# Optimization experiments

Measured on AMD Instinct MI355X. Metric: run time of the kernel, lower is better.

The kernel has to match this reference:

```python
import jax, jax.numpy as jnp
import numpy as np

N, E, IN, H, OUT, L = 50000, 640000, 64, 128, 128, 4
EPS = 1e-8


def setup_inputs() -> dict:
    key = jax.random.key(0)
    ks = jax.random.split(key, 14)
    rn = lambda k, shp: (jax.random.normal(k, shp, jnp.float32) * 0.05)
    return {
        "h": jax.random.normal(ks[0], (N, IN), jnp.float32),
        "pos": jax.random.normal(ks[1], (N, 3), jnp.float32),
        "edge_index": jax.random.randint(ks[2], (2, E), 0, N),
        "emb_W": rn(ks[3], (IN, H)), "emb_b": jnp.zeros((H,), jnp.float32),
        "msg_W1": rn(ks[4], (L, 2 * H + 1, H)), "msg_b1": jnp.zeros((L, H), jnp.float32),
        "msg_W2": rn(ks[5], (L, H, H)), "msg_b2": jnp.zeros((L, H), jnp.float32),
        "coord_W1": rn(ks[6], (L, H, H)), "coord_b1": jnp.zeros((L, H), jnp.float32),
        "coord_W2": rn(ks[7], (L, H, 1)), "coord_b2": jnp.zeros((L, 1), jnp.float32),
        "node_W1": rn(ks[8], (L, 2 * H, H)), "node_b1": jnp.zeros((L, H), jnp.float32),
        "node_W2": rn(ks[9], (L, H, H)), "node_b2": jnp.zeros((L, H), jnp.float32),
        "out_W1": rn(ks[10], (H, H)), "out_b1": jnp.zeros((H,), jnp.float32),
        "out_W2": rn(ks[11], (H, OUT)), "out_b2": jnp.zeros((OUT,), jnp.float32),
    }


def _egnn_forward(h, pos, src, dst, emb_W, emb_b, msg_W1, msg_b1, msg_W2, msg_b2,
                  coord_W1, coord_b1, coord_W2, coord_b2, node_W1, node_b1,
                  node_W2, node_b2, out_W1, out_b1, out_W2, out_b2):
    n = h.shape[0]
    h = h @ emb_W + emb_b  # node embedding [N, H]
    for l in range(L):
        hi, hj = h[dst], h[src]                     # target i, source j gathers [Etot, H]
        rel = pos[src] - pos[dst]                   # row - col (used for coord update)
        dist = jnp.linalg.norm(rel, axis=-1, keepdims=True)  # symmetric, same as |pos_i - pos_j|
        # message MLP: Linear -> SiLU -> Linear -> SiLU on [h_i, h_j, dist]
        m = jax.nn.silu(jnp.concatenate([hi, hj, dist], axis=-1) @ msg_W1[l] + msg_b1[l])
        m = jax.nn.silu(m @ msg_W2[l] + msg_b2[l])
        agg = jax.ops.segment_sum(m, dst, num_segments=n)  # scatter-add to targets
        # coord update: weights from h[row]=h_j, scatter to col=dst
        w = jax.nn.silu(hj @ coord_W1[l] + coord_b1[l]) @ coord_W2[l] + coord_b2[l]  # [Etot,1]
        coord_diff = w * rel / (dist + EPS)
        pos = pos + jax.ops.segment_sum(coord_diff, dst, num_segments=n)
        # node update with residual
        nh = jax.nn.silu(jnp.concatenate([h, agg], axis=-1) @ node_W1[l] + node_b1[l]) @ node_W2[l] + node_b2[l]
        h = h + nh
    out = jax.nn.silu(h @ out_W1 + out_b1) @ out_W2 + out_b2
    return out, pos


def reference(h, pos, edge_index, emb_W, emb_b, msg_W1, msg_b1, msg_W2, msg_b2,
              coord_W1, coord_b1, coord_W2, coord_b2, node_W1, node_b1,
              node_W2, node_b2, out_W1, out_b1, out_W2, out_b2):
    n = h.shape[0]
    loops = jnp.arange(n)  # add_self_loops
    src = jnp.concatenate([edge_index[0], loops])
    dst = jnp.concatenate([edge_index[1], loops])
    return _egnn_forward(h, pos, src, dst, emb_W, emb_b, msg_W1, msg_b1, msg_W2,
                         msg_b2, coord_W1, coord_b1, coord_W2, coord_b2, node_W1,
                         node_b1, node_W2, node_b2, out_W1, out_b1, out_W2, out_b2)
```

## Files before the change

### kernel.cpp

```cpp
#include <hip/hip_runtime.h>
#include <hip/hip_bf16.h>

#define EPSV 1e-8f

typedef short bf16x8 __attribute__((ext_vector_type(8)));
typedef float f32x4  __attribute__((ext_vector_type(4)));

__device__ __forceinline__ float silu_f(float x) {
    return x * __builtin_amdgcn_rcpf(1.0f + __expf(-x));
}
__device__ __forceinline__ float bf2f(short v) {
    return __uint_as_float(((unsigned int)(unsigned short)v) << 16);
}
__device__ __forceinline__ short f2bfs(float f) {
    __hip_bfloat16 h = __float2bfloat16(f);
    return *(short*)&h;
}

#define MAXM 24
struct PackArgs {
    const float* src[MAXM];
    unsigned int doff[MAXM];
    int nchunk[MAXM];
    int nmat;
};

__global__ __launch_bounds__(256) void repack_kernel(PackArgs pa, __hip_bfloat16* base)
{
    int bid = blockIdx.x;
    int m = 0, c = bid;
    while (m < pa.nmat && c >= pa.nchunk[m]) { c -= pa.nchunk[m]; ++m; }
    const float* src = pa.src[m];
    __hip_bfloat16* dst = base + pa.doff[m] + (size_t)c * 4096;
    for (int o = threadIdx.x; o < 4096; o += 256) {
        int j = o & 7, n = (o >> 3) & 127, g = o >> 10;
        dst[o] = __float2bfloat16(src[(size_t)(c * 32 + g * 8 + j) * 128 + n]);
    }
}

__global__ __launch_bounds__(256) void hist_kernel(
    const int* __restrict__ ei, int* __restrict__ cnt, int E, int N)
{
    int e = blockIdx.x * 256 + threadIdx.x;
    int Etot = E + N;
    if (e < Etot) {
        int d = (e < E) ? ei[E + e] : (e - E);
        atomicAdd(&cnt[d], 1);
    }
}

__global__ __launch_bounds__(256) void scan_block_kernel(
    const int* __restrict__ cnt, int* __restrict__ off, int* __restrict__ part, int n)
{
    __shared__ int sdata[256];
    const int tid = threadIdx.x;
    const int base = blockIdx.x * 4096 + tid * 16;
    int loc[16]; int s = 0;
    #pragma unroll
    for (int i = 0; i < 16; ++i) {
        int idx = base + i;
        int v = (idx < n) ? cnt[idx] : 0;
        loc[i] = s; s += v;
    }
    sdata[tid] = s;
    __syncthreads();
    for (int st = 1; st < 256; st <<= 1) {
        int v = (tid >= st) ? sdata[tid - st] : 0;
        __syncthreads();
        sdata[tid] += v;
        __syncthreads();
    }
    int texc = (tid > 0) ? sdata[tid - 1] : 0;
    #pragma unroll
    for (int i = 0; i < 16; ++i) {
        int idx = base + i;
        if (idx < n) off[idx] = texc + loc[i];
    }
    if (tid == 255) part[blockIdx.x] = sdata[255];
}

__global__ void scan_part_kernel(int* part, int np)
{
    if (threadIdx.x == 0 && blockIdx.x == 0) {
        int run = 0;
        for (int i = 0; i < np; ++i) { int v = part[i]; part[i] = run; run += v; }
    }
}

__global__ __launch_bounds__(256) void scan_add_kernel(
    int* __restrict__ off, const int* __restrict__ part, int n)
{
    int idx = blockIdx.x * 4096 + threadIdx.x * 16;
    int p = part[blockIdx.x];
    #pragma unroll
    for (int i = 0; i < 16; ++i)
        if (idx + i < n) off[idx + i] += p;
}

__global__ __launch_bounds__(256) void scatter_kernel(
    const int* __restrict__ ei, int* __restrict__ off,
    int* __restrict__ esrc, int* __restrict__ edst, int E, int N)
{
    int e = blockIdx.x * 256 + threadIdx.x;
    int Etot = E + N;
    if (e < Etot) {
        int s, d;
        if (e < E) { s = ei[e]; d = ei[E + e]; }
        else       { s = d = e - E; }
        int p = atomicAdd(&off[d], 1);
        esrc[p] = s; edst[p] = d;
    }
}

template<int LDA>
__device__ __forceinline__ void mfma_gemm(const __hip_bfloat16 (*At)[LDA], int acol0,
                                          const __hip_bfloat16* __restrict__ Bp,
                                          int kchunks, int w, int lane, f32x4 acc[4][2])
{
    const int ar = lane & 15, g = lane >> 4;
    const int bc = w * 32 + (lane & 15);
    for (int c = 0; c < kchunks; ++c) {
        const int ao = acol0 + c * 32 + g * 8;
        bf16x8 a0 = *(const bf16x8*)&At[ar +  0][ao];
        bf16x8 a1 = *(const bf16x8*)&At[ar + 16][ao];
        bf16x8 a2 = *(const bf16x8*)&At[ar + 32][ao];
        bf16x8 a3 = *(const bf16x8*)&At[ar + 48][ao];
        const __hip_bfloat16* bb = Bp + ((size_t)((c * 4 + g) * 128) + bc) * 8;
        bf16x8 b0 = *(const bf16x8*)(bb);
        bf16x8 b1 = *(const bf16x8*)(bb + 128);
        acc[0][0] = __builtin_amdgcn_mfma_f32_16x16x32_bf16(a0, b0, acc[0][0], 0, 0, 0);
        acc[1][0] = __builtin_amdgcn_mfma_f32_16x16x32_bf16(a1, b0, acc[1][0], 0, 0, 0);
        acc[2][0] = __builtin_amdgcn_mfma_f32_16x16x32_bf16(a2, b0, acc[2][0], 0, 0, 0);
        acc[3][0] = __builtin_amdgcn_mfma_f32_16x16x32_bf16(a3, b0, acc[3][0], 0, 0, 0);
        acc[0][1] = __builtin_amdgcn_mfma_f32_16x16x32_bf16(a0, b1, acc[0][1], 0, 0, 0);
        acc[1][1] = __builtin_amdgcn_mfma_f32_16x16x32_bf16(a1, b1, acc[1][1], 0, 0, 0);
        acc[2][1] = __builtin_amdgcn_mfma_f32_16x16x32_bf16(a2, b1, acc[2][1], 0, 0, 0);
        acc[3][1] = __builtin_amdgcn_mfma_f32_16x16x32_bf16(a3, b1, acc[3][1], 0, 0, 0);
    }
}

__device__ __forceinline__ void zacc(f32x4 acc[4][2]) {
    #pragma unroll
    for (int r = 0; r < 4; ++r)
        #pragma unroll
        for (int c = 0; c < 2; ++c) acc[r][c] = (f32x4){0.f, 0.f, 0.f, 0.f};
}

__global__ __launch_bounds__(256) void embed_pre_kernel(
    const float* __restrict__ hin,
    const __hip_bfloat16* __restrict__ embWp, const float* __restrict__ embb,
    const __hip_bfloat16* __restrict__ W1p, const float* __restrict__ b1,
    const __hip_bfloat16* __restrict__ cW1p,
    const float* __restrict__ cb1, const float* __restrict__ cW2,
    const float* __restrict__ cb2,
    float* __restrict__ hbuf, __hip_bfloat16* __restrict__ h16,
    __hip_bfloat16* __restrict__ U16, __hip_bfloat16* __restrict__ V16,
    float* __restrict__ wnum, int N)
{
    __shared__ __hip_bfloat16 a_e[64][72];
    __shared__ __hip_bfloat16 a_h[64][136];
    __shared__ float redw[64][4];
    const int t = threadIdx.x;
    const int nb = blockIdx.x * 64;
    const int lane = t & 63, w = t >> 6, g = lane >> 4, l15 = lane & 15;

    #pragma unroll
    for (int it = 0; it < 2; ++it) {
        int flat = t + 256 * it;
        int c8 = flat & 7, e = flat >> 3;
        int node = nb + e; if (node >= N) node = N - 1;
        const float* hp = hin + (size_t)node * 64 + c8 * 8;
        float4 v0 = *(const float4*)hp, v1 = *(const float4*)(hp + 4);
        bf16x8 r;
        r[0] = f2bfs(v0.x); r[1] = f2bfs(v0.y); r[2] = f2bfs(v0.z); r[3] = f2bfs(v0.w);
        r[4] = f2bfs(v1.x); r[5] = f2bfs(v1.y); r[6] = f2bfs(v1.z); r[7] = f2bfs(v1.w);
        *(bf16x8*)(&a_e[e][c8 * 8]) = r;
    }
    __syncthreads();

    const int colA = w * 32 + l15, colB = colA + 16;
    f32x4 acc[4][2];

    zacc(acc);
    mfma_gemm<72>(a_e, 0, embWp, 2, w, lane, acc);
    {
        float bA = embb[colA], bB = embb[colB];
        #pragma unroll
        for (int r = 0; r < 4; ++r)
            #pragma unroll
            for (int q = 0; q < 4; ++q) {
                int row = r * 16 + g * 4 + q;
                int node = nb + row;
                float va = acc[r][0][q] + bA, vb = acc[r][1][q] + bB;
                __hip_bfloat16 ha = __float2bfloat16(va), hb = __float2bfloat16(vb);
                a_h[row][colA] = ha; a_h[row][colB] = hb;
                if (node < N) {
                    size_t off = (size_t)node * 128;
                    hbuf[off + colA] = va; hbuf[off + colB] = vb;
                    h16[off + colA] = ha; h16[off + colB] = hb;
                }
            }
    }
    __syncthreads();

    zacc(acc);
    mfma_gemm<136>(a_h, 0, W1p, 4, w, lane, acc);
    {
        float bA = b1[colA], bB = b1[colB];
        #pragma unroll
        for (int r = 0; r < 4; ++r)
            #pragma unroll
            for (int q = 0; q < 4; ++q) {
                int node = nb + r * 16 + g * 4 + q;
                if (node < N) {
                    U16[(size_t)node * 128 + colA] = __float2bfloat16(acc[r][0][q] + bA);
                    U16[(size_t)node * 128 + colB] = __float2bfloat16(acc[r][1][q] + bB);
                }
            }
    }
    zacc(acc);
    mfma_gemm<136>(a_h, 0, W1p + 4 * 4096, 4, w, lane, acc);
    #pragma unroll
    for (int r = 0; r < 4; ++r)
        #pragma unroll
        for (int q = 0; q < 4; ++q) {
            int node = nb + r * 16 + g * 4 + q;
            if (node < N) {
                V16[(size_t)node * 128 + colA] = __float2bfloat16(acc[r][0][q]);
                V16[(size_t)node * 128 + colB] = __float2bfloat16(acc[r][1][q]);
            }
        }
    zacc(acc);
    mfma_gemm<136>(a_h, 0, cW1p, 4, w, lane, acc);
    {
        float cb1A = cb1[colA], cb1B = cb1[colB];
        float wA = cW2[colA], wB = cW2[colB];
        #pragma unroll
        for (int r = 0; r < 4; ++r)
            #pragma unroll
            for (int q = 0; q < 4; ++q) {
                float p = silu_f(acc[r][0][q] + cb1A) * wA
                        + silu_f(acc[r][1][q] + cb1B) * wB;
                p += __shfl_xor(p, 1);
                p += __shfl_xor(p, 2);
                p += __shfl_xor(p, 4);
                p += __shfl_xor(p, 8);
                if (l15 == 0) redw[r * 16 + g * 4 + q][w] = p;
            }
    }
    __syncthreads();
    if (t < 64 && nb + t < N)
        wnum[nb + t] = redw[t][0] + redw[t][1] + redw[t][2] + redw[t][3] + cb2[0];
}

__global__ __launch_bounds__(256) void edge_kernel(
    const __hip_bfloat16* __restrict__ U16, const __hip_bfloat16* __restrict__ V16,
    const float* __restrict__ wnum, const float* __restrict__ posb,
    const int* __restrict__ esrc, const int* __restrict__ edst,
    const float* __restrict__ W1tail,
    const __hip_bfloat16* __restrict__ W2p, const float* __restrict__ b2,
    float* __restrict__ agg, float* __restrict__ pdel, int Etot)
{
    __shared__ __hip_bfloat16 m1s[64][136];
    __shared__ int   dstl[64];
    __shared__ float relt[3][64], distl[64], wscl[64];

    const int t = threadIdx.x;
    const int eb = blockIdx.x * 64;
    const int lane = t & 63, w = t >> 6, g = lane >> 4, l15 = lane & 15;

    const int c8 = t & 15, row0 = t >> 4;
    bf16x8 uvr[4], vvr[4];
    int dval[4];
    #pragma unroll
    for (int j = 0; j < 4; ++j) {
        int row = row0 + 16 * j;
        int e = eb + row;
        int s = 0, d = 0;
        if (e < Etot) { s = esrc[e]; d = edst[e]; dval[j] = 1; }
        else          { dval[j] = 0; }
        uvr[j] = *(const bf16x8*)(U16 + (size_t)d * 128 + c8 * 8);
        vvr[j] = *(const bf16x8*)(V16 + (size_t)s * 128 + c8 * 8);
    }

    if (t < 64) {
        int e = eb + t;
        int s = 0, d = -1;
        if (e < Etot) { s = esrc[e]; d = edst[e]; }
        dstl[t] = d;
        int dd = (d < 0) ? 0 : d;
        float rx = posb[3 * s + 0] - posb[3 * dd + 0];
        float ry = posb[3 * s + 1] - posb[3 * dd + 1];
        float rz = posb[3 * s + 2] - posb[3 * dd + 2];
        float dist = sqrtf(rx * rx + ry * ry + rz * rz);
        relt[0][t] = rx; relt[1][t] = ry; relt[2][t] = rz;
        distl[t] = dist;
        wscl[t] = wnum[s] * __builtin_amdgcn_rcpf(dist + EPSV);
    }
    __syncthreads();

    if (t < 192) {
        int e = t / 3, comp = t % 3;
        if (dstl[e] >= 0)
            atomicAdd(&pdel[(size_t)dstl[e] * 3 + comp], wscl[e] * relt[comp][e]);
    }

    {
        float wt[8];
        *(float4*)&wt[0] = *(const float4*)(W1tail + c8 * 8);
        *(float4*)&wt[4] = *(const float4*)(W1tail + c8 * 8 + 4);
        #pragma unroll
        for (int j = 0; j < 4; ++j) {
            int row = row0 + 16 * j;
            bf16x8 res;
            if (dval[j]) {
                float dv = distl[row];
                #pragma unroll
                for (int k = 0; k < 8; ++k) {
                    float x = bf2f(uvr[j][k]) + bf2f(vvr[j][k]) + dv * wt[k];
                    res[k] = f2bfs(silu_f(x));
                }
            } else {
                #pragma unroll
                for (int k = 0; k < 8; ++k) res[k] = 0;
            }
            *(bf16x8*)(&m1s[row][c8 * 8]) = res;
        }
    }
    __syncthreads();

    const int colA = w * 32 + l15, colB = colA + 16;
    f32x4 acc[4][2];
    zacc(acc);
    mfma_gemm<136>(m1s, 0, W2p, 4, w, lane, acc);
    __syncthreads();

    {
        float b2a = b2[colA], b2b = b2[colB];
        #pragma unroll
        for (int r = 0; r < 4; ++r)
            #pragma unroll
            for (int q = 0; q < 4; ++q) {
                int row = r * 16 + g * 4 + q;
                m1s[row][colA] = __float2bfloat16(silu_f(acc[r][0][q] + b2a));
                m1s[row][colB] = __float2bfloat16(silu_f(acc[r][1][q] + b2b));
            }
    }
    __syncthreads();

    {
        int col = t & 127, half = t >> 7;
        int r0 = half * 32;
        float a = 0.f;
        int cur = dstl[r0];
        #pragma unroll 4
        for (int r = r0; r < r0 + 32; ++r) {
            int d = dstl[r];
            if (d != cur) {
                if (cur >= 0) atomicAdd(&agg[(size_t)cur * 128 + col], a);
                a = 0.f; cur = d;
            }
            if (d >= 0) a += bf2f(*(const short*)&m1s[r][col]);
        }
        if (cur >= 0) atomicAdd(&agg[(size_t)cur * 128 + col], a);
    }
}

__global__ __launch_bounds__(256) void node_mfma_kernel(
    float* __restrict__ hbuf, __hip_bfloat16* __restrict__ h16,
    const float* __restrict__ agg,
    float* __restrict__ posb, const float* __restrict__ pdel,
    const __hip_bfloat16* __restrict__ W1p, const float* __restrict__ b1,
    const __hip_bfloat16* __restrict__ W2p, const float* __restrict__ b2,
    const __hip_bfloat16* __restrict__ nxtW1p, const float* __restrict__ nxt_b1,
    const __hip_bfloat16* __restrict__ nxt_cW1p, const float* __restrict__ nxt_cb1,
    const float* __restrict__ nxt_cW2, const float* __restrict__ nxt_cb2,
    __hip_bfloat16* __restrict__ U16, __hip_bfloat16* __restrict__ V16,
    float* __restrict__ wnum,
    const __hip_bfloat16* __restrict__ oW1p, const float* __restrict__ ob1,
    const __hip_bfloat16* __restrict__ oW2p, const float* __restrict__ ob2,
    float* __restrict__ outp,
    int N, int mode)
{
    __shared__ __hip_bfloat16 a_t[64][264];
    __shared__ __hip_bfloat16 us[64][136];
    __shared__ float redw[64][4];
    const int t = threadIdx.x;
    const int nb = blockIdx.x * 64;
    const int lane = t & 63, w = t >> 6, g = lane >> 4, l15 = lane & 15;

    #pragma unroll
    for (int it = 0; it < 4; ++it) {
        int flat = t + 256 * it;
        int c = flat & 15, e = flat >> 4;
        int node = nb + e; if (node >= N) node = N - 1;
        *(int4*)(&a_t[e][c * 8]) = *(const int4*)(h16 + (size_t)node * 128 + c * 8);
    }
    #pragma unroll
    for (int it = 0; it < 8; ++it) {
        int flat = t + 256 * it;
        int c = flat & 31, e = flat >> 5;
        int node = nb + e; if (node >= N) node = N - 1;
        float4 v = *(const float4*)(agg + (size_t)node * 128 + c * 4);
        __hip_bfloat16* p = &a_t[e][128 + c * 4];
        p[0] = __float2bfloat16(v.x); p[1] = __float2bfloat16(v.y);
        p[2] = __float2bfloat16(v.z); p[3] = __float2bfloat16(v.w);
    }
    __syncthreads();

    const int colA = w * 32 + l15, colB = colA + 16;
    f32x4 acc[4][2];

    zacc(acc);
    mfma_gemm<264>(a_t, 0, W1p, 8, w, lane, acc);
    {
        float b1a = b1[colA], b1b = b1[colB];
        #pragma unroll
        for (int r = 0; r < 4; ++r)
            #pragma unroll
            for (int q = 0; q < 4; ++q) {
                int row = r * 16 + g * 4 + q;
                us[row][colA] = __float2bfloat16(silu_f(acc[r][0][q] + b1a));
                us[row][colB] = __float2bfloat16(silu_f(acc[r][1][q] + b1b));
            }
    }
    __syncthreads();

    zacc(acc);
    mfma_gemm<136>(us, 0, W2p, 4, w, lane, acc);
    {
        float b2a = b2[colA], b2b = b2[colB];
        #pragma unroll
        for (int r = 0; r < 4; ++r)
            #pragma unroll
            for (int q = 0; q < 4; ++q) {
                int row = r * 16 + g * 4 + q;
                int node = nb + row;
                if (node < N) {
                    size_t off = (size_t)node * 128;
                    float va = hbuf[off + colA] + acc[r][0][q] + b2a;
                    float vb = hbuf[off + colB] + acc[r][1][q] + b2b;
                    hbuf[off + colA] = va; hbuf[off + colB] = vb;
                    __hip_bfloat16 ha = __float2bfloat16(va), hb = __float2bfloat16(vb);
                    h16[off + colA] = ha; h16[off + colB] = hb;
                    a_t[row][colA] = ha; a_t[row][colB] = hb;
                } else {
                    a_t[row][colA] = __float2bfloat16(0.f);
                    a_t[row][colB] = __float2bfloat16(0.f);
                }
            }
    }
    if (t < 192) {
        int e = t / 3, comp = t % 3;
        int node = nb + e;
        if (node < N) posb[3 * node + comp] += pdel[3 * node + comp];
    }

    if (mode == 0) return;
    __syncthreads();

    if (mode == 2) {
        zacc(acc);
        mfma_gemm<264>(a_t, 0, oW1p, 4, w, lane, acc);
        {
            float b1a = ob1[colA], b1b = ob1[colB];
            #pragma unroll
            for (int r = 0; r < 4; ++r)
                #pragma unroll
                for (int q = 0; q < 4; ++q) {
                    int row = r * 16 + g * 4 + q;
                    us[row][colA] = __float2bfloat16(silu_f(acc[r][0][q] + b1a));
                    us[row][colB] = __float2bfloat16(silu_f(acc[r][1][q] + b1b));
                }
        }
        __syncthreads();
        zacc(acc);
        mfma_gemm<136>(us, 0, oW2p, 4, w, lane, acc);
        {
            float b2a = ob2[colA], b2b = ob2[colB];
            #pragma unroll
            for (int r = 0; r < 4; ++r)
                #pragma unroll
                for (int q = 0; q < 4; ++q) {
                    int row = r * 16 + g * 4 + q;
                    int node = nb + row;
                    if (node < N) {
                        outp[(size_t)node * 128 + colA] = acc[r][0][q] + b2a;
                        outp[(size_t)node * 128 + colB] = acc[r][1][q] + b2b;
                    }
                }
        }
        return;
    }

    zacc(acc);
    mfma_gemm<264>(a_t, 0, nxtW1p, 4, w, lane, acc);
    {
        float bA = nxt_b1[colA], bB = nxt_b1[colB];
        #pragma unroll
        for (int r = 0; r < 4; ++r)
            #pragma unroll
            for (int q = 0; q < 4; ++q) {
                int node = nb + r * 16 + g * 4 + q;
                if (node < N) {
                    U16[(size_t)node * 128 + colA] = __float2bfloat16(acc[r][0][q] + bA);
                    U16[(size_t)node * 128 + colB] = __float2bfloat16(acc[r][1][q] + bB);
                }
            }
    }
    zacc(acc);
    mfma_gemm<264>(a_t, 0, nxtW1p + 4 * 4096, 4, w, lane, acc);
    #pragma unroll
    for (int r = 0; r < 4; ++r)
        #pragma unroll
        for (int q = 0; q < 4; ++q) {
            int node = nb + r * 16 + g * 4 + q;
            if (node < N) {
                V16[(size_t)node * 128 + colA] = __float2bfloat16(acc[r][0][q]);
                V16[(size_t)node * 128 + colB] = __float2bfloat16(acc[r][1][q]);
            }
        }
    zacc(acc);
    mfma_gemm<264>(a_t, 0, nxt_cW1p, 4, w, lane, acc);
    {
        float cb1A = nxt_cb1[colA], cb1B = nxt_cb1[colB];
        float wA = nxt_cW2[colA], wB = nxt_cW2[colB];
        #pragma unroll
        for (int r = 0; r < 4; ++r)
            #pragma unroll
            for (int q = 0; q < 4; ++q) {
                float p = silu_f(acc[r][0][q] + cb1A) * wA
                        + silu_f(acc[r][1][q] + cb1B) * wB;
                p += __shfl_xor(p, 1);
                p += __shfl_xor(p, 2);
                p += __shfl_xor(p, 4);
                p += __shfl_xor(p, 8);
                if (l15 == 0) redw[r * 16 + g * 4 + q][w] = p;
            }
    }
    __syncthreads();
    if (t < 64 && nb + t < N)
        wnum[nb + t] = redw[t][0] + redw[t][1] + redw[t][2] + redw[t][3] + nxt_cb2[0];
}

extern "C" void kernel_launch(void* const* d_in, const int* in_sizes, int n_in,
                              void* d_out, int out_size, void* d_ws, size_t ws_size,
                              hipStream_t stream)
{
    const float* hin  = (const float*)d_in[0];
    const float* pos  = (const float*)d_in[1];
    const int*   ei   = (const int*)d_in[2];
    const float* embW = (const float*)d_in[3];
    const float* embb = (const float*)d_in[4];
    const float* mW1  = (const float*)d_in[5];
    const float* mb1  = (const float*)d_in[6];
    const float* mW2  = (const float*)d_in[7];
    const float* mb2  = (const float*)d_in[8];
    const float* cW1  = (const float*)d_in[9];
    const float* cb1  = (const float*)d_in[10];
    const float* cW2  = (const float*)d_in[11];
    const float* cb2  = (const float*)d_in[12];
    const float* nW1  = (const float*)d_in[13];
    const float* nb1  = (const float*)d_in[14];
    const float* nW2  = (const float*)d_in[15];
    const float* nb2  = (const float*)d_in[16];
    const float* oW1  = (const float*)d_in[17];
    const float* ob1  = (const float*)d_in[18];
    const float* oW2  = (const float*)d_in[19];
    const float* ob2  = (const float*)d_in[20];

    const int N = in_sizes[0] / 64;
    const int E = in_sizes[2] / 2;
    const int Etot = E + N;

    float* hbuf = (float*)d_ws;
    float* aggb = hbuf + (size_t)N * 128;
    float* posb = aggb + (size_t)N * 128;
    float* pdel = posb + (size_t)N * 3;
    float* wnum = pdel + (size_t)N * 3;
    __hip_bfloat16* h16 = (__hip_bfloat16*)(wnum + N);
    __hip_bfloat16* U16 = h16 + (size_t)N * 128;
    __hip_bfloat16* V16 = U16 + (size_t)N * 128;
    __hip_bfloat16* packed = V16 + (size_t)N * 128;
    int* cnt  = (int*)(packed + 122 * 4096);
    int* soff = cnt + N;
    int* part = soff + N;
    int* esrc = part + 64;
    int* edst = esrc + Etot;
    float* outp = (float*)d_out;

    PackArgs pa;
    int nm = 0; unsigned int poff = 0; int totalChunks = 0;
    auto addm = [&](const float* s, int kc) {
        pa.src[nm] = s; pa.doff[nm] = poff; pa.nchunk[nm] = kc;
        poff += (unsigned int)kc * 4096; totalChunks += kc; ++nm;
    };
    for (int l = 0; l < 4; ++l) {
        addm(mW1 + (size_t)l * 257 * 128, 8);
        addm(mW2 + (size_t)l * 128 * 128, 4);
        addm(cW1 + (size_t)l * 128 * 128, 4);
        addm(nW1 + (size_t)l * 256 * 128, 8);
        addm(nW2 + (size_t)l * 128 * 128, 4);
    }
    addm(oW1, 4);
    addm(oW2, 4);
    addm(embW, 2);
    pa.nmat = nm;

    const unsigned int LSTRIDE = 28 * 4096;
    const __hip_bfloat16* oW1p  = packed + (size_t)4 * LSTRIDE;
    const __hip_bfloat16* oW2p  = packed + (size_t)4 * LSTRIDE + 4 * 4096;
    const __hip_bfloat16* embWp = packed + (size_t)4 * LSTRIDE + 8 * 4096;

    hipMemcpyAsync(posb, pos, (size_t)N * 3 * sizeof(float),
                   hipMemcpyDeviceToDevice, stream);
    repack_kernel<<<totalChunks, 256, 0, stream>>>(pa, packed);

    const int scanBlocks = (N + 4095) / 4096;
    hipMemsetAsync(cnt, 0, (size_t)N * sizeof(int), stream);
    hist_kernel<<<(Etot + 255) / 256, 256, 0, stream>>>(ei, cnt, E, N);
    scan_block_kernel<<<scanBlocks, 256, 0, stream>>>(cnt, soff, part, N);
    scan_part_kernel<<<1, 64, 0, stream>>>(part, scanBlocks);
    scan_add_kernel<<<scanBlocks, 256, 0, stream>>>(soff, part, N);
    scatter_kernel<<<(Etot + 255) / 256, 256, 0, stream>>>(ei, soff, esrc, edst, E, N);

    const int nodeBlocks64 = (N + 63) / 64;
    const int edgeBlocks   = (Etot + 63) / 64;

    embed_pre_kernel<<<nodeBlocks64, 256, 0, stream>>>(
        hin, embWp, embb,
        packed, mb1, packed + 12 * 4096,
        cb1, cW2, cb2,
        hbuf, h16, U16, V16, wnum, N);

    for (int l = 0; l < 4; ++l) {
        hipMemsetAsync(aggb, 0, (size_t)N * 128 * sizeof(float), stream);
        hipMemsetAsync(pdel, 0, (size_t)N * 3 * sizeof(float), stream);
        const __hip_bfloat16* lp = packed + (size_t)l * LSTRIDE;
        edge_kernel<<<edgeBlocks, 256, 0, stream>>>(
            U16, V16, wnum, posb, esrc, edst,
            mW1 + (size_t)l * 257 * 128 + 256 * 128,
            lp + 8 * 4096, mb2 + l * 128,
            aggb, pdel, Etot);
        const int ln = (l < 3) ? (l + 1) : l;
        const __hip_bfloat16* lpn = packed + (size_t)ln * LSTRIDE;
        node_mfma_kernel<<<nodeBlocks64, 256, 0, stream>>>(
            hbuf, h16, aggb, posb, pdel,
            lp + 16 * 4096, nb1 + l * 128,
            lp + 24 * 4096, nb2 + l * 128,
            lpn, mb1 + (size_t)ln * 128,
            lpn + 12 * 4096, cb1 + (size_t)ln * 128,
            cW2 + (size_t)ln * 128, cb2 + ln,
            U16, V16, wnum,
            oW1p, ob1, oW2p, ob2, outp,
            N, (l < 3) ? 1 : 2);
    }

    hipMemcpyAsync(outp + (size_t)N * 128, posb, (size_t)N * 3 * sizeof(float),
                   hipMemcpyDeviceToDevice, stream);
}
```

Baseline: 1.025 ms.

## Drop fp32 hidden-state buffer and restructure edge gather to use staged indices

```diff
diff --git a/kernel.cpp b/kernel.cpp
--- a/kernel.cpp
+++ b/kernel.cpp
@@ -153,7 +153,7 @@
     const __hip_bfloat16* __restrict__ cW1p,
     const float* __restrict__ cb1, const float* __restrict__ cW2,
     const float* __restrict__ cb2,
-    float* __restrict__ hbuf, __hip_bfloat16* __restrict__ h16,
+    __hip_bfloat16* __restrict__ h16,
     __hip_bfloat16* __restrict__ U16, __hip_bfloat16* __restrict__ V16,
     float* __restrict__ wnum, int N)
 {
@@ -196,7 +196,6 @@
                 a_h[row][colA] = ha; a_h[row][colB] = hb;
                 if (node < N) {
                     size_t off = (size_t)node * 128;
-                    hbuf[off + colA] = va; hbuf[off + colB] = vb;
                     h16[off + colA] = ha; h16[off + colB] = hb;
                 }
             }
@@ -262,32 +261,18 @@
     float* __restrict__ agg, float* __restrict__ pdel, int Etot)
 {
     __shared__ __hip_bfloat16 m1s[64][136];
-    __shared__ int   dstl[64];
+    __shared__ int   srcl[64], dstl[64];
     __shared__ float relt[3][64], distl[64], wscl[64];
 
     const int t = threadIdx.x;
     const int eb = blockIdx.x * 64;
     const int lane = t & 63, w = t >> 6, g = lane >> 4, l15 = lane & 15;
-
-    const int c8 = t & 15, row0 = t >> 4;
-    bf16x8 uvr[4], vvr[4];
-    int dval[4];
-    #pragma unroll
-    for (int j = 0; j < 4; ++j) {
-        int row = row0 + 16 * j;
-        int e = eb + row;
-        int s = 0, d = 0;
-        if (e < Etot) { s = esrc[e]; d = edst[e]; dval[j] = 1; }
-        else          { dval[j] = 0; }
-        uvr[j] = *(const bf16x8*)(U16 + (size_t)d * 128 + c8 * 8);
-        vvr[j] = *(const bf16x8*)(V16 + (size_t)s * 128 + c8 * 8);
-    }
 
     if (t < 64) {
         int e = eb + t;
         int s = 0, d = -1;
         if (e < Etot) { s = esrc[e]; d = edst[e]; }
-        dstl[t] = d;
+        srcl[t] = s; dstl[t] = d;
         int dd = (d < 0) ? 0 : d;
         float rx = posb[3 * s + 0] - posb[3 * dd + 0];
         float ry = posb[3 * s + 1] - posb[3 * dd + 1];
@@ -299,33 +284,29 @@
     }
     __syncthreads();
 
-    if (t < 192) {
-        int e = t / 3, comp = t % 3;
-        if (dstl[e] >= 0)
-            atomicAdd(&pdel[(size_t)dstl[e] * 3 + comp], wscl[e] * relt[comp][e]);
-    }
-
-    {
-        float wt[8];
-        *(float4*)&wt[0] = *(const float4*)(W1tail + c8 * 8);
-        *(float4*)&wt[4] = *(const float4*)(W1tail + c8 * 8 + 4);
-        #pragma unroll
-        for (int j = 0; j < 4; ++j) {
-            int row = row0 + 16 * j;
-            bf16x8 res;
-            if (dval[j]) {
-                float dv = distl[row];
-                #pragma unroll
-                for (int k = 0; k < 8; ++k) {
-                    float x = bf2f(uvr[j][k]) + bf2f(vvr[j][k]) + dv * wt[k];
-                    res[k] = f2bfs(silu_f(x));
-                }
-            } else {
-                #pragma unroll
-                for (int k = 0; k < 8; ++k) res[k] = 0;
-            }
-            *(bf16x8*)(&m1s[row][c8 * 8]) = res;
+    #pragma unroll
+    for (int j = 0; j < 4; ++j) {
+        int f = t + 256 * j;
+        int c8 = f & 15, row = f >> 4;
+        bf16x8 res;
+        if (dstl[row] >= 0) {
+            int s = srcl[row], d = dstl[row];
+            bf16x8 uv = *(const bf16x8*)(U16 + (size_t)d * 128 + c8 * 8);
+            bf16x8 vv = *(const bf16x8*)(V16 + (size_t)s * 128 + c8 * 8);
+            float wt[8];
+            *(float4*)&wt[0] = *(const float4*)(W1tail + c8 * 8);
+            *(float4*)&wt[4] = *(const float4*)(W1tail + c8 * 8 + 4);
+            float dv = distl[row];
+            #pragma unroll
+            for (int k = 0; k < 8; ++k) {
+                float x = bf2f(uv[k]) + bf2f(vv[k]) + dv * wt[k];
+                res[k] = f2bfs(silu_f(x));
+            }
+        } else {
+            #pragma unroll
+            for (int k = 0; k < 8; ++k) res[k] = 0;
         }
+        *(bf16x8*)(&m1s[row][c8 * 8]) = res;
     }
     __syncthreads();
 
@@ -364,10 +345,16 @@
         }
         if (cur >= 0) atomicAdd(&agg[(size_t)cur * 128 + col], a);
     }
+
+    if (t < 192) {
+        int e = t / 3, comp = t % 3;
+        if (dstl[e] >= 0)
+            atomicAdd(&pdel[(size_t)dstl[e] * 3 + comp], wscl[e] * relt[comp][e]);
+    }
 }
 
 __global__ __launch_bounds__(256) void node_mfma_kernel(
-    float* __restrict__ hbuf, __hip_bfloat16* __restrict__ h16,
+    __hip_bfloat16* __restrict__ h16,
     const float* __restrict__ agg,
     float* __restrict__ posb, const float* __restrict__ pdel,
     const __hip_bfloat16* __restrict__ W1p, const float* __restrict__ b1,
@@ -438,9 +425,8 @@
                 int node = nb + row;
                 if (node < N) {
                     size_t off = (size_t)node * 128;
-                    float va = hbuf[off + colA] + acc[r][0][q] + b2a;
-                    float vb = hbuf[off + colB] + acc[r][1][q] + b2b;
-                    hbuf[off + colA] = va; hbuf[off + colB] = vb;
+                    float va = bf2f(*(const short*)&a_t[row][colA]) + acc[r][0][q] + b2a;
+                    float vb = bf2f(*(const short*)&a_t[row][colB]) + acc[r][1][q] + b2b;
                     __hip_bfloat16 ha = __float2bfloat16(va), hb = __float2bfloat16(vb);
                     h16[off + colA] = ha; h16[off + colB] = hb;
                     a_t[row][colA] = ha; a_t[row][colB] = hb;
@@ -573,8 +559,7 @@
     const int E = in_sizes[2] / 2;
     const int Etot = E + N;
 
-    float* hbuf = (float*)d_ws;
-    float* aggb = hbuf + (size_t)N * 128;
+    float* aggb = (float*)d_ws;
     float* posb = aggb + (size_t)N * 128;
     float* pdel = posb + (size_t)N * 3;
     float* wnum = pdel + (size_t)N * 3;
@@ -631,7 +616,7 @@
         hin, embWp, embb,
         packed, mb1, packed + 12 * 4096,
         cb1, cW2, cb2,
-        hbuf, h16, U16, V16, wnum, N);
+        h16, U16, V16, wnum, N);
 
     for (int l = 0; l < 4; ++l) {
         hipMemsetAsync(aggb, 0, (size_t)N * 128 * sizeof(float), stream);
@@ -645,7 +630,7 @@
         const int ln = (l < 3) ? (l + 1) : l;
         const __hip_bfloat16* lpn = packed + (size_t)ln * LSTRIDE;
         node_mfma_kernel<<<nodeBlocks64, 256, 0, stream>>>(
-            hbuf, h16, aggb, posb, pdel,
+            h16, aggb, posb, pdel,
             lp + 16 * 4096, nb1 + l * 128,
             lp + 24 * 4096, nb2 + l * 128,
             lpn, mb1 + (size_t)ln * 128,
```

Result: faster. 1.004 ms (-2.0%).
